# Kernel optimization log

Hardware: AMD Instinct MI355X
Metric: run time of the kernel (lower is better)

The kernel has to match this reference:

```python
import jax, jax.numpy as jnp
import numpy as np

MARGIN = 0.5  # init kwarg: margin=0.5, adaptive_margin=True


def setup_inputs() -> dict:
    key = jax.random.key(0)
    k1, k2 = jax.random.split(key)
    B, D, N_CLASSES = 8192, 128, 128
    return {
        "embeddings": jax.random.normal(k1, (B, D), dtype=jnp.float32),
        "labels": jax.random.randint(k2, (B,), 0, N_CLASSES),
    }


def _distance_matrix(e):
    # add 1e-16 where exactly zero, sqrt, then zero those entries back out.
    dot = e @ e.T                      # [B, B]
    sq = jnp.diagonal(dot)             # [B]
    d2 = jax.nn.relu(sq[None, :] - 2.0 * dot + sq[:, None])
    zmask = (d2 == 0.0).astype(e.dtype)
    return jnp.sqrt(d2 + zmask * 1e-16) * (1.0 - zmask)


def reference(embeddings, labels):
    B = embeddings.shape[0]
    # F.normalize(p=2, dim=1) with eps clamp
    norm = jnp.maximum(jnp.linalg.norm(embeddings, axis=1, keepdims=True), 1e-12)
    e = embeddings / norm
    d = _distance_matrix(e)            # [B, B]

    eq = labels[:, None] == labels[None, :]
    eye = jnp.eye(B, dtype=bool)
    pos_mask = eq & ~eye               # same-label, excluding self
    neg_mask = ~eq                     # different-label (diag auto-excluded)

    BIG = jnp.asarray(1e9, d.dtype)
    hardest_pos = jnp.max(jnp.where(pos_mask, d, -BIG), axis=1)  # [B]
    hardest_neg = jnp.min(jnp.where(neg_mask, d, BIG), axis=1)   # [B]
    valid = pos_mask.any(axis=1) & neg_mask.any(axis=1)

    # torch uses .item() -> margin is a constant w.r.t. autodiff
    adaptive_margin = MARGIN * (1.0 + jax.lax.stop_gradient(hardest_pos))
    per_row = jax.nn.relu(hardest_pos - hardest_neg + adaptive_margin)
    per_row = jnp.where(valid, per_row, 0.0)
    count = jnp.maximum(jnp.sum(valid.astype(d.dtype)), 1.0)
    return jnp.sum(per_row) / count
```

## Files before the change

kernel.cpp:

```cpp
#include <hip/hip_runtime.h>

#define BN   8192
#define DIM  128
#define NCLS 128
#define NBLK 1024
#define NSTR 4

typedef __attribute__((ext_vector_type(8))) short bf16x8;
typedef __attribute__((ext_vector_type(8))) unsigned short u16x8;
typedef __attribute__((ext_vector_type(4))) float f32x4;

static __device__ __forceinline__ unsigned short f2bf(float x) {
    union { float f; unsigned u; } c; c.f = x;
    unsigned r = c.u + 0x7FFFu + ((c.u >> 16) & 1u);
    return (unsigned short)(r >> 16);
}

static __device__ __forceinline__ bf16x8 ldb8(const unsigned short* p) {
    return *reinterpret_cast<const bf16x8*>(p);
}

static __device__ __forceinline__ unsigned encf(float f) {
    unsigned u = __float_as_uint(f);
    return (u >> 31) ? ~u : (u | 0x80000000u);
}
static __device__ __forceinline__ float decf(unsigned v) {
    return __uint_as_float((v >> 31) ? (v & 0x7FFFFFFFu) : ~v);
}

static __device__ __forceinline__ void gload_lds16(const unsigned short* g, unsigned short* l) {
    __builtin_amdgcn_global_load_lds(
        (const __attribute__((address_space(1))) unsigned int*)g,
        (__attribute__((address_space(3))) unsigned int*)l, 16, 0, 0);
}

__global__ __launch_bounds__(256) void sort_norm(const float* __restrict__ emb,
                                                 const int* __restrict__ labels,
                                                 unsigned short* __restrict__ ebf,
                                                 int2* __restrict__ se,
                                                 unsigned* __restrict__ hp2,
                                                 unsigned* __restrict__ hn2) {
    const int c   = blockIdx.x;
    const int tid = threadIdx.x;
    __shared__ int slab[BN];
    __shared__ int sl[256], so[256];
    __shared__ int srcrow[512];

#pragma unroll 8
    for (int k = 0; k < 32; ++k) {
        int idx = k * 256 + tid;
        slab[idx] = labels[idx];
    }
    __syncthreads();

    int nl = 0, no = 0;
#pragma unroll 8
    for (int k = 0; k < 32; ++k) {
        int lb = slab[k * 256 + tid];
        nl += (lb < c);
        no += (lb == c);
    }
    sl[tid] = nl; so[tid] = no;
    __syncthreads();
    for (int off = 1; off < 256; off <<= 1) {
        int a1 = 0, a2 = 0;
        if (tid >= off) { a1 = sl[tid - off]; a2 = so[tid - off]; }
        __syncthreads();
        sl[tid] += a1; so[tid] += a2;
        __syncthreads();
    }
    const int offs_c = sl[255];
    const int n_c    = so[255];
    int mypos = so[tid] - no;
    for (int k = 0; k < 32; ++k) {
        int r = k * 256 + tid;
        if (slab[r] == c) srcrow[mypos++] = r;
    }
    __syncthreads();

    const int grp = tid >> 4;
    const int gl  = tid & 15;
    for (int k = grp; k < n_c; k += 16) {
        const int r   = srcrow[k];
        const int pos = offs_c + k;
        const float4* rp = reinterpret_cast<const float4*>(emb + (size_t)r * DIM);
        float4 v0 = rp[gl * 2];
        float4 v1 = rp[gl * 2 + 1];
        float ss = v0.x * v0.x + v0.y * v0.y + v0.z * v0.z + v0.w * v0.w
                 + v1.x * v1.x + v1.y * v1.y + v1.z * v1.z + v1.w * v1.w;
#pragma unroll
        for (int m = 1; m < 16; m <<= 1) ss += __shfl_xor(ss, m);
        float inv = 1.0f / fmaxf(sqrtf(ss), 1e-12f);
        u16x8 bv;
        bv[0] = f2bf(v0.x * inv); bv[1] = f2bf(v0.y * inv);
        bv[2] = f2bf(v0.z * inv); bv[3] = f2bf(v0.w * inv);
        bv[4] = f2bf(v1.x * inv); bv[5] = f2bf(v1.y * inv);
        bv[6] = f2bf(v1.z * inv); bv[7] = f2bf(v1.w * inv);
        *reinterpret_cast<u16x8*>(ebf + (size_t)pos * DIM + gl * 8) = bv;
        if (gl == 0) {
            se[pos]  = make_int2(offs_c, offs_c + n_c);
            hp2[pos] = 0xFFFFFFFFu;
            hn2[pos] = 0u;
        }
    }
}

__global__ __launch_bounds__(256) void tri_main(const unsigned short* __restrict__ ebf,
                                                const int2* __restrict__ se,
                                                unsigned* __restrict__ hp2,
                                                unsigned* __restrict__ hn2) {
    __shared__ alignas(16) unsigned short as_[2][64 * DIM];

    const int tid  = threadIdx.x;
    const int wave = tid >> 6;
    const int lane = tid & 63;
    const int lr   = lane & 15;
    const int lk   = lane >> 4;
    const int jb   = blockIdx.x >> 5;
    const int isp  = blockIdx.x & 31;
    const int jc0  = jb * 256 + wave * 64;
    const int rb0  = isp * 256;

    bf16x8 b[4][4];
#pragma unroll
    for (int cs = 0; cs < 4; ++cs)
#pragma unroll
        for (int kk = 0; kk < 4; ++kk)
            b[cs][kk] = ldb8(ebf + (size_t)(jc0 + cs * 16 + lr) * DIM + kk * 32 + lk * 8);

    int qs[4], qe[4];
#pragma unroll
    for (int cs = 0; cs < 4; ++cs) {
        int2 q = se[jc0 + cs * 16 + lr];
        qs[cs] = q.x; qe[cs] = q.y;
    }

    float hp[4] = {1e30f, 1e30f, 1e30f, 1e30f};
    float hn[4] = {-1e30f, -1e30f, -1e30f, -1e30f};

    int perm[4];
#pragma unroll
    for (int kk = 0; kk < 4; ++kk) perm[kk] = ((kk * 4 + lk) ^ (lr & 7)) << 4;

    const int rloc  = lane >> 4;
    const int chunk = lane & 15;
    auto STAGE = [&](int buf, int s) {
        const unsigned short* g0 = ebf + (size_t)(rb0 + s * 64) * DIM;
        unsigned short* lb = &as_[buf][wave * 16 * DIM];
#pragma unroll
        for (int l = 0; l < 4; ++l) {
            const int row = l * 4 + rloc;
            gload_lds16(g0 + (size_t)(wave * 16 + row) * DIM + ((chunk ^ (row & 7)) * 8),
                        lb + l * 4 * DIM);
        }
    };

    STAGE(0, 0);
    __syncthreads();

    for (int s = 0; s < NSTR; ++s) {
        if (s < NSTR - 1) STAGE((s + 1) & 1, s + 1);

        const char* bb = reinterpret_cast<const char*>(&as_[s & 1][0]);
        f32x4 acc[4][4];
#pragma unroll
        for (int cs = 0; cs < 4; ++cs)
#pragma unroll
            for (int t = 0; t < 4; ++t) acc[cs][t] = f32x4{0.f, 0.f, 0.f, 0.f};

#pragma unroll
        for (int t = 0; t < 4; ++t)
#pragma unroll
            for (int kk = 0; kk < 4; ++kk) {
                bf16x8 af = *reinterpret_cast<const bf16x8*>(bb + (t * 16 + lr) * 256 + perm[kk]);
                acc[0][t] = __builtin_amdgcn_mfma_f32_16x16x32_bf16(af, b[0][kk], acc[0][t], 0, 0, 0);
                acc[1][t] = __builtin_amdgcn_mfma_f32_16x16x32_bf16(af, b[1][kk], acc[1][t], 0, 0, 0);
                acc[2][t] = __builtin_amdgcn_mfma_f32_16x16x32_bf16(af, b[2][kk], acc[2][t], 0, 0, 0);
                acc[3][t] = __builtin_amdgcn_mfma_f32_16x16x32_bf16(af, b[3][kk], acc[3][t], 0, 0, 0);
            }

        const int rb = rb0 + s * 64;
        bool mixed = false;
#pragma unroll
        for (int cs = 0; cs < 4; ++cs)
            mixed |= (qs[cs] < rb + 64) && (qe[cs] > rb);

        if (!__any(mixed)) {
#pragma unroll
            for (int cs = 0; cs < 4; ++cs) {
                float mx = hn[cs];
#pragma unroll
                for (int t = 0; t < 4; ++t)
#pragma unroll
                    for (int m = 0; m < 4; ++m) mx = fmaxf(mx, acc[cs][t][m]);
                hn[cs] = mx;
            }
        } else {
#pragma unroll
            for (int cs = 0; cs < 4; ++cs)
#pragma unroll
                for (int t = 0; t < 4; ++t)
#pragma unroll
                    for (int m = 0; m < 4; ++m) {
                        const int rowg = rb + t * 16 + lk * 4 + m;
                        const float d = acc[cs][t][m];
                        const bool pos = (rowg >= qs[cs]) && (rowg < qe[cs]);
                        hp[cs] = pos ? fminf(hp[cs], d) : hp[cs];
                        hn[cs] = pos ? hn[cs] : fmaxf(hn[cs], d);
                    }
        }

        __syncthreads();
    }

#pragma unroll
    for (int cs = 0; cs < 4; ++cs) {
#pragma unroll
        for (int sft = 16; sft < 64; sft <<= 1) {
            hp[cs] = fminf(hp[cs], __shfl_xor(hp[cs], sft));
            hn[cs] = fmaxf(hn[cs], __shfl_xor(hn[cs], sft));
        }
    }
    if (lane < 16) {
#pragma unroll
        for (int cs = 0; cs < 4; ++cs) {
            atomicMin(&hp2[jc0 + cs * 16 + lane], encf(hp[cs]));
            atomicMax(&hn2[jc0 + cs * 16 + lane], encf(hn[cs]));
        }
    }
}

__global__ __launch_bounds__(1024) void finalize_kernel(const unsigned* __restrict__ hp2,
                                                        const unsigned* __restrict__ hn2,
                                                        float* __restrict__ out) {
    const int tid = threadIdx.x;
    float sum = 0.f;
#pragma unroll
    for (int it = 0; it < BN / (1024 * 4); ++it) {
        int base = (it * 1024 + tid) * 4;
        uint4 pv = *reinterpret_cast<const uint4*>(&hp2[base]);
        uint4 nv = *reinterpret_cast<const uint4*>(&hn2[base]);
        unsigned pa[4] = {pv.x, pv.y, pv.z, pv.w};
        unsigned na[4] = {nv.x, nv.y, nv.z, nv.w};
#pragma unroll
        for (int e = 0; e < 4; ++e) {
            float pd = decf(pa[e]);
            float nd = decf(na[e]);
            float hpv = sqrtf(fmaxf(2.0f - 2.0f * pd, 0.f));
            float hnv = sqrtf(fmaxf(2.0f - 2.0f * nd, 0.f));
            sum += fmaxf(fmaf(1.5f, hpv, 0.5f) - hnv, 0.f);
        }
    }
    __shared__ float red[1024];
    red[tid] = sum;
    __syncthreads();
    for (int s2 = 512; s2 > 0; s2 >>= 1) {
        if (tid < s2) red[tid] += red[tid + s2];
        __syncthreads();
    }
    if (tid == 0) out[0] = red[0] * (1.0f / (float)BN);
}

extern "C" void kernel_launch(void* const* d_in, const int* in_sizes, int n_in,
                              void* d_out, int out_size, void* d_ws, size_t ws_size,
                              hipStream_t stream) {
    const float* emb    = (const float*)d_in[0];
    const int*   labels = (const int*)d_in[1];
    float* out = (float*)d_out;

    char* ws = (char*)d_ws;
    unsigned short* ebf = (unsigned short*)ws;
    int2*     se   = (int2*)    (ws + 2u * 1024u * 1024u);
    unsigned* hp2  = (unsigned*)(ws + 2u * 1024u * 1024u + 64u * 1024u);
    unsigned* hn2  = (unsigned*)(ws + 2u * 1024u * 1024u + 96u * 1024u);

    hipLaunchKernelGGL(sort_norm,       dim3(NCLS), dim3(256),  0, stream, emb, labels, ebf, se, hp2, hn2);
    hipLaunchKernelGGL(tri_main,        dim3(NBLK), dim3(256),  0, stream, ebf, se, hp2, hn2);
    hipLaunchKernelGGL(finalize_kernel, dim3(1),    dim3(1024), 0, stream, hp2, hn2, out);
}
```

Before: 45.51 us.

## Load row tiles directly from global into registers instead of LDS staging

Removes the double-buffered LDS staging of 64-row A tiles (global_load_lds plus barriers). Each wave now loads its 16-row A fragments straight from global/L2 into registers, 16 rows per iteration, and the mask checks run at 16-row granularity. This drops LDS traffic and the per-stage __syncthreads. In exchange, all four waves redundantly fetch the same A rows from cache, there is less latency hiding, and the MFMA chains per iteration are shorter.

```diff
diff --git a/kernel.cpp b/kernel.cpp
--- a/kernel.cpp
+++ b/kernel.cpp
@@ -4,7 +4,6 @@
 #define DIM  128
 #define NCLS 128
 #define NBLK 1024
-#define NSTR 4
 
 typedef __attribute__((ext_vector_type(8))) short bf16x8;
 typedef __attribute__((ext_vector_type(8))) unsigned short u16x8;
@@ -26,12 +25,6 @@
 }
 static __device__ __forceinline__ float decf(unsigned v) {
     return __uint_as_float((v >> 31) ? (v & 0x7FFFFFFFu) : ~v);
-}
-
-static __device__ __forceinline__ void gload_lds16(const unsigned short* g, unsigned short* l) {
-    __builtin_amdgcn_global_load_lds(
-        (const __attribute__((address_space(1))) unsigned int*)g,
-        (__attribute__((address_space(3))) unsigned int*)l, 16, 0, 0);
 }
 
 __global__ __launch_bounds__(256) void sort_norm(const float* __restrict__ emb,
@@ -109,8 +102,6 @@
                                                 const int2* __restrict__ se,
                                                 unsigned* __restrict__ hp2,
                                                 unsigned* __restrict__ hn2) {
-    __shared__ alignas(16) unsigned short as_[2][64 * DIM];
-
     const int tid  = threadIdx.x;
     const int wave = tid >> 6;
     const int lane = tid & 63;
@@ -138,79 +129,51 @@
     float hp[4] = {1e30f, 1e30f, 1e30f, 1e30f};
     float hn[4] = {-1e30f, -1e30f, -1e30f, -1e30f};
 
-    int perm[4];
-#pragma unroll
-    for (int kk = 0; kk < 4; ++kk) perm[kk] = ((kk * 4 + lk) ^ (lr & 7)) << 4;
-
-    const int rloc  = lane >> 4;
-    const int chunk = lane & 15;
-    auto STAGE = [&](int buf, int s) {
-        const unsigned short* g0 = ebf + (size_t)(rb0 + s * 64) * DIM;
-        unsigned short* lb = &as_[buf][wave * 16 * DIM];
-#pragma unroll
-        for (int l = 0; l < 4; ++l) {
-            const int row = l * 4 + rloc;
-            gload_lds16(g0 + (size_t)(wave * 16 + row) * DIM + ((chunk ^ (row & 7)) * 8),
-                        lb + l * 4 * DIM);
-        }
-    };
-
-    STAGE(0, 0);
-    __syncthreads();
-
-    for (int s = 0; s < NSTR; ++s) {
-        if (s < NSTR - 1) STAGE((s + 1) & 1, s + 1);
-
-        const char* bb = reinterpret_cast<const char*>(&as_[s & 1][0]);
-        f32x4 acc[4][4];
+#pragma unroll 2
+    for (int rt = 0; rt < 16; ++rt) {
+        const int rb = rb0 + rt * 16;
+        const unsigned short* ap = ebf + (size_t)(rb + lr) * DIM + lk * 8;
+        bf16x8 a0 = ldb8(ap);
+        bf16x8 a1 = ldb8(ap + 32);
+        bf16x8 a2 = ldb8(ap + 64);
+        bf16x8 a3 = ldb8(ap + 96);
+
+        f32x4 acc[4];
+#pragma unroll
+        for (int cs = 0; cs < 4; ++cs) acc[cs] = f32x4{0.f, 0.f, 0.f, 0.f};
+#pragma unroll
+        for (int cs = 0; cs < 4; ++cs) {
+            acc[cs] = __builtin_amdgcn_mfma_f32_16x16x32_bf16(a0, b[cs][0], acc[cs], 0, 0, 0);
+            acc[cs] = __builtin_amdgcn_mfma_f32_16x16x32_bf16(a1, b[cs][1], acc[cs], 0, 0, 0);
+            acc[cs] = __builtin_amdgcn_mfma_f32_16x16x32_bf16(a2, b[cs][2], acc[cs], 0, 0, 0);
+            acc[cs] = __builtin_amdgcn_mfma_f32_16x16x32_bf16(a3, b[cs][3], acc[cs], 0, 0, 0);
+        }
+
+        bool mixed = false;
 #pragma unroll
         for (int cs = 0; cs < 4; ++cs)
-#pragma unroll
-            for (int t = 0; t < 4; ++t) acc[cs][t] = f32x4{0.f, 0.f, 0.f, 0.f};
-
-#pragma unroll
-        for (int t = 0; t < 4; ++t)
-#pragma unroll
-            for (int kk = 0; kk < 4; ++kk) {
-                bf16x8 af = *reinterpret_cast<const bf16x8*>(bb + (t * 16 + lr) * 256 + perm[kk]);
-                acc[0][t] = __builtin_amdgcn_mfma_f32_16x16x32_bf16(af, b[0][kk], acc[0][t], 0, 0, 0);
-                acc[1][t] = __builtin_amdgcn_mfma_f32_16x16x32_bf16(af, b[1][kk], acc[1][t], 0, 0, 0);
-                acc[2][t] = __builtin_amdgcn_mfma_f32_16x16x32_bf16(af, b[2][kk], acc[2][t], 0, 0, 0);
-                acc[3][t] = __builtin_amdgcn_mfma_f32_16x16x32_bf16(af, b[3][kk], acc[3][t], 0, 0, 0);
-            }
-
-        const int rb = rb0 + s * 64;
-        bool mixed = false;
-#pragma unroll
-        for (int cs = 0; cs < 4; ++cs)
-            mixed |= (qs[cs] < rb + 64) && (qe[cs] > rb);
+            mixed |= (qs[cs] < rb + 16) && (qe[cs] > rb);
 
         if (!__any(mixed)) {
 #pragma unroll
             for (int cs = 0; cs < 4; ++cs) {
                 float mx = hn[cs];
 #pragma unroll
-                for (int t = 0; t < 4; ++t)
-#pragma unroll
-                    for (int m = 0; m < 4; ++m) mx = fmaxf(mx, acc[cs][t][m]);
+                for (int m = 0; m < 4; ++m) mx = fmaxf(mx, acc[cs][m]);
                 hn[cs] = mx;
             }
         } else {
 #pragma unroll
             for (int cs = 0; cs < 4; ++cs)
 #pragma unroll
-                for (int t = 0; t < 4; ++t)
-#pragma unroll
-                    for (int m = 0; m < 4; ++m) {
-                        const int rowg = rb + t * 16 + lk * 4 + m;
-                        const float d = acc[cs][t][m];
-                        const bool pos = (rowg >= qs[cs]) && (rowg < qe[cs]);
-                        hp[cs] = pos ? fminf(hp[cs], d) : hp[cs];
-                        hn[cs] = pos ? hn[cs] : fmaxf(hn[cs], d);
-                    }
-        }
-
-        __syncthreads();
+                for (int m = 0; m < 4; ++m) {
+                    const int rowg = rb + lk * 4 + m;
+                    const float d = acc[cs][m];
+                    const bool pos = (rowg >= qs[cs]) && (rowg < qe[cs]);
+                    hp[cs] = pos ? fminf(hp[cs], d) : hp[cs];
+                    hn[cs] = pos ? hn[cs] : fmaxf(hn[cs], d);
+                }
+        }
     }
 
 #pragma unroll
```

Result: slower. 65.25 us (+43.4%).
